# Kernel tuning notes

Hardware: AMD Instinct MI355X
Metric: run time of the kernel (lower is better)

The kernel has to match this reference:

```python
import jax, jax.numpy as jnp
import numpy as np

SEQ_LEN = 181
N_FEAT = 12
N_EMB = 128
N_LAYER = 2
BATCH = 4096


def setup_inputs() -> dict:
    key = jax.random.key(0)
    ks = jax.random.split(key, 13)
    s = 0.05  # small init scale, typical of trained recurrent weights
    H, F = N_EMB, N_FEAT
    return {
        "enc_h": jax.random.normal(ks[0], (N_LAYER, BATCH, H), jnp.float32),
        "enc_c": jax.random.normal(ks[1], (N_LAYER, BATCH, H), jnp.float32),
        "Wih0": jax.random.normal(ks[2], (4 * H, H), jnp.float32) * s,
        "Whh0": jax.random.normal(ks[3], (4 * H, H), jnp.float32) * s,
        "bih0": jax.random.normal(ks[4], (4 * H,), jnp.float32) * s,
        "bhh0": jax.random.normal(ks[5], (4 * H,), jnp.float32) * s,
        "Wih1": jax.random.normal(ks[6], (4 * H, H), jnp.float32) * s,
        "Whh1": jax.random.normal(ks[7], (4 * H, H), jnp.float32) * s,
        "bih1": jax.random.normal(ks[8], (4 * H,), jnp.float32) * s,
        "bhh1": jax.random.normal(ks[9], (4 * H,), jnp.float32) * s,
        "Wout": jax.random.normal(ks[10], (F, N_LAYER * H), jnp.float32) * s,
        "bout": jax.random.normal(ks[11], (F,), jnp.float32) * s,
    }


def _lstm_cell(x, h, c, Wih, Whh, bih, bhh):
    # PyTorch gate order: i, f, g, o
    g = x @ Wih.T + bih + h @ Whh.T + bhh  # (N, 4H)
    i, f, gg, o = jnp.split(g, 4, axis=-1)
    c = jax.nn.sigmoid(f) * c + jax.nn.sigmoid(i) * jnp.tanh(gg)
    h = jax.nn.sigmoid(o) * jnp.tanh(c)
    return h, c


def reference(enc_h, enc_c, Wih0, Whh0, bih0, bhh0, Wih1, Whh1, bih1, bhh1, Wout, bout):
    N, H = enc_h.shape[1], enc_h.shape[2]
    layers = ((Wih0, Whh0, bih0, bhh0), (Wih1, Whh1, bih1, bhh1))

    def lstm2(x_seq, h, c):
        # x_seq: (N, 2, H) batch_first; h, c: (2, N, H)
        inp = x_seq
        hs, cs = [], []
        for l, (Wih, Whh, bih, bhh) in enumerate(layers):
            hl, cl = h[l], c[l]
            outs = []
            for t in range(N_LAYER):  # the fake 'sequence' length equals n_layer=2
                hl, cl = _lstm_cell(inp[:, t], hl, cl, Wih, Whh, bih, bhh)
                outs.append(hl)
            inp = jnp.stack(outs, axis=1)  # (N, 2, H)
            hs.append(hl)
            cs.append(cl)
        return inp, jnp.stack(hs), jnp.stack(cs)

    def step(carry, _):
        dec_in, h, c = carry
        oi, h, c = lstm2(dec_in, h, c)
        out = jax.nn.sigmoid(oi.reshape(N, -1) @ Wout.T + bout)  # (N, n_feat)
        return (oi, h, c), out

    dec_in0 = jnp.zeros((N, N_LAYER, H), enc_h.dtype)
    _, outs = jax.lax.scan(step, (dec_in0, enc_h, enc_c), None, length=SEQ_LEN)
    return jnp.transpose(outs, (1, 0, 2))  # (N, seq_len, n_feat)
```

## Files before the change

### kernel.cpp

```cpp
#include <hip/hip_runtime.h>
#include <hip/hip_bf16.h>

typedef __attribute__((ext_vector_type(8))) short bf16x8;
typedef __attribute__((ext_vector_type(4))) float f32x4;

#define NBATCH 4096
#define SEQT 181
#define NFEAT 12
#define HDIM 128
#define ROWS 16
#define LSTR 136
#define OUTSTRIDE (SEQT*NFEAT)

#define WFRAG_ELEMS 262144
#define WOUT_ELEMS  4096
#define BIAS_F32OFF (532480/4)
#define BOUT_F32OFF (536576/4)
#define BBF16_U16OFF 268320

#define ACT_OFF  131072
#define BIAS_OFF 157184
#define BOUT_OFF 161280
#define SMEM_BYTES 161344

#define SSIG (-1.442695041f)
#define STANH (-2.885390082f)

#define FBAR() asm volatile("s_waitcnt lgkmcnt(0)\n\ts_barrier" ::: "memory")

__device__ __forceinline__ float fsig2(float xs) {
  return __builtin_amdgcn_rcpf(1.0f + __builtin_amdgcn_exp2f(xs));
}
__device__ __forceinline__ unsigned short f2bf(float x) {
  __hip_bfloat16 h = __float2bfloat16(x);
  return __builtin_bit_cast(unsigned short, h);
}

__global__ void setup_kernel(const float* __restrict__ Wih0, const float* __restrict__ Whh0,
                             const float* __restrict__ bih0, const float* __restrict__ bhh0,
                             const float* __restrict__ Wih1, const float* __restrict__ Whh1,
                             const float* __restrict__ bih1, const float* __restrict__ bhh1,
                             const float* __restrict__ Wo,   const float* __restrict__ bo,
                             unsigned short* __restrict__ ws)
{
  int idx = blockIdx.x * blockDim.x + threadIdx.x;
  if (idx < WFRAG_ELEMS) {
    int e = idx & 7, lane = (idx >> 3) & 63, s = (idx >> 9) & 7, g = (idx >> 12) & 3,
        w = (idx >> 14) & 7, l = idx >> 17;
    int row = g * 128 + w * 16 + (lane & 15);
    int k   = s * 32 + (lane >> 4) * 8 + e;
    const float* Wih = l ? Wih1 : Wih0;
    const float* Whh = l ? Whh1 : Whh0;
    float v = (k < HDIM) ? Wih[row * HDIM + k] : Whh[row * HDIM + (k - HDIM)];
    float sc = (g == 2) ? STANH : SSIG;
    ws[idx] = f2bf(v * sc);
  } else if (idx < WFRAG_ELEMS + WOUT_ELEMS) {
    int i2 = idx - WFRAG_ELEMS;
    int e = i2 & 7, lane = (i2 >> 3) & 63, s = i2 >> 9;
    int c = lane & 15;
    int k = s * 32 + (lane >> 4) * 8 + e;
    float v = (c < NFEAT) ? Wo[c * 256 + k] * SSIG : 0.0f;
    ws[idx] = f2bf(v);
  } else if (idx < WFRAG_ELEMS + WOUT_ELEMS + 1024) {
    int i3 = idx - (WFRAG_ELEMS + WOUT_ELEMS);
    int l = i3 >> 9, r = i3 & 511;
    float v = l ? (bih1[r] + bhh1[r]) : (bih0[r] + bhh0[r]);
    reinterpret_cast<float*>(ws)[BIAS_F32OFF + i3] = v;
  } else if (idx < WFRAG_ELEMS + WOUT_ELEMS + 1024 + 16) {
    int i4 = idx - (WFRAG_ELEMS + WOUT_ELEMS + 1024);
    reinterpret_cast<float*>(ws)[BOUT_F32OFF + i4] = (i4 < NFEAT) ? bo[i4] * SSIG : 0.0f;
  } else if (idx < WFRAG_ELEMS + WOUT_ELEMS + 1024 + 16 + 1024) {
    int i5 = idx - (WFRAG_ELEMS + WOUT_ELEMS + 1024 + 16);
    int l = i5 >> 9, r = i5 & 511;
    int w = r >> 6, lg = (r >> 4) & 3, j16 = r & 15;
    int f = j16 >> 3, j = j16 & 7;
    int gate = f * 2 + (j >> 2);
    int dim  = w * 16 + lg * 4 + (j & 3);
    float v = l ? (bih1[gate * 128 + dim] + bhh1[gate * 128 + dim])
                : (bih0[gate * 128 + dim] + bhh0[gate * 128 + dim]);
    float sc = (gate == 2) ? STANH : SSIG;
    ws[BBF16_U16OFF + i5] = f2bf(v * sc);
  }
}

__global__ void
__attribute__((amdgpu_flat_work_group_size(512, 512), amdgpu_waves_per_eu(2, 2)))
lstm_kernel(
    const float* __restrict__ ench, const float* __restrict__ encc,
    const unsigned short* __restrict__ wfrag, const unsigned short* __restrict__ woutf,
    const unsigned short* __restrict__ biasbf, const float* __restrict__ boutc,
    float* __restrict__ out)
{
  __shared__ __align__(16) unsigned char smem[SMEM_BYTES];
  bf16x8* wlds = reinterpret_cast<bf16x8*>(smem);
  unsigned short* act = reinterpret_cast<unsigned short*>(smem + ACT_OFF);

  const int tid  = threadIdx.x;
  const int wave = tid >> 6, lane = tid & 63;
  const int col  = lane & 15, lg = lane >> 4;
  const int n0   = blockIdx.x * ROWS;
  const int dbase = wave * 16 + lg * 4;

  const bf16x8* wfv = reinterpret_cast<const bf16x8*>(wfrag);

  bf16x8 wreg[2][4][6];
  #pragma unroll
  for (int l = 0; l < 2; ++l)
    #pragma unroll
    for (int g = 0; g < 4; ++g) {
      #pragma unroll
      for (int s = 0; s < 6; ++s)
        wreg[l][g][s] = wfv[(size_t)((((l * 8 + wave) * 4 + g) * 8) + s) * 64 + lane];
      #pragma unroll
      for (int s = 0; s < 6; ++s) {
        f32x4 t_ = __builtin_bit_cast(f32x4, wreg[l][g][s]);
        asm volatile("" : "+v"(t_));
        wreg[l][g][s] = __builtin_bit_cast(bf16x8, t_);
      }
      __builtin_amdgcn_sched_barrier(0);
    }

  #pragma unroll
  for (int l = 0; l < 2; ++l)
    #pragma unroll
    for (int g = 0; g < 4; ++g)
      #pragma unroll
      for (int si = 0; si < 2; ++si)
        wlds[(((wave * 2 + l) * 4 + g) * 2 + si) * 64 + lane] =
            wfv[(size_t)((((l * 8 + wave) * 4 + g) * 8) + 6 + si) * 64 + lane];

  for (int i = tid; i < 2 * ROWS * LSTR; i += 512) act[i] = 0;
  for (int i = tid; i < ROWS * HDIM; i += 512) {
    int r = i >> 7, d = i & (HDIM - 1);
    act[(5 * ROWS + r) * LSTR + d] = f2bf(ench[(n0 + r) * HDIM + d]);
    act[(3 * ROWS + r) * LSTR + d] = f2bf(ench[(size_t)(NBATCH + n0 + r) * HDIM + d]);
  }
  for (int i = tid; i < 1024; i += 512)
    reinterpret_cast<unsigned short*>(smem + BIAS_OFF)[i] = biasbf[i];
  if (tid < 16) reinterpret_cast<float*>(smem + BOUT_OFF)[tid] = boutc[tid];
  f32x4 c0 = *reinterpret_cast<const f32x4*>(&encc[(size_t)(n0 + col) * HDIM + dbase]);
  f32x4 c1 = *reinterpret_cast<const f32x4*>(&encc[(size_t)(NBATCH + n0 + col) * HDIM + dbase]);
  __syncthreads();

  const int aoffl = col * LSTR + lg * 8;

  auto cellNB = [&](int xb, int hb, int ob, const bf16x8 (&wr)[4][6], int lb, int bl, f32x4& c) {
    const unsigned short* xp = act + xb * (ROWS * LSTR) + aoffl;
    const unsigned short* hp = act + hb * (ROWS * LSTR) + aoffl;
    const unsigned char* bptr = smem + BIAS_OFF + (size_t)(((bl * 8 + wave) * 4 + lg) * 32);
    bf16x8 bb0 = *reinterpret_cast<const bf16x8*>(bptr);
    bf16x8 bb1 = *reinterpret_cast<const bf16x8*>(bptr + 16);
    f32x4 acc0, acc1, acc2, acc3;
    #pragma unroll
    for (int j = 0; j < 4; ++j) {
      acc0[j] = __builtin_bit_cast(float, ((unsigned)(unsigned short)bb0[j]) << 16);
      acc1[j] = __builtin_bit_cast(float, ((unsigned)(unsigned short)bb0[4 + j]) << 16);
      acc2[j] = __builtin_bit_cast(float, ((unsigned)(unsigned short)bb1[j]) << 16);
      acc3[j] = __builtin_bit_cast(float, ((unsigned)(unsigned short)bb1[4 + j]) << 16);
    }
    #pragma unroll
    for (int s = 0; s < 4; ++s) {
      bf16x8 b = *reinterpret_cast<const bf16x8*>(&xp[s * 32]);
      acc0 = __builtin_amdgcn_mfma_f32_16x16x32_bf16(wr[0][s], b, acc0, 0, 0, 0);
      acc1 = __builtin_amdgcn_mfma_f32_16x16x32_bf16(wr[1][s], b, acc1, 0, 0, 0);
      acc2 = __builtin_amdgcn_mfma_f32_16x16x32_bf16(wr[2][s], b, acc2, 0, 0, 0);
      acc3 = __builtin_amdgcn_mfma_f32_16x16x32_bf16(wr[3][s], b, acc3, 0, 0, 0);
    }
    #pragma unroll
    for (int s = 0; s < 2; ++s) {
      bf16x8 b = *reinterpret_cast<const bf16x8*>(&hp[s * 32]);
      acc0 = __builtin_amdgcn_mfma_f32_16x16x32_bf16(wr[0][4 + s], b, acc0, 0, 0, 0);
      acc1 = __builtin_amdgcn_mfma_f32_16x16x32_bf16(wr[1][4 + s], b, acc1, 0, 0, 0);
      acc2 = __builtin_amdgcn_mfma_f32_16x16x32_bf16(wr[2][4 + s], b, acc2, 0, 0, 0);
      acc3 = __builtin_amdgcn_mfma_f32_16x16x32_bf16(wr[3][4 + s], b, acc3, 0, 0, 0);
    }
    #pragma unroll
    for (int si = 0; si < 2; ++si) {
      bf16x8 b = *reinterpret_cast<const bf16x8*>(&hp[(2 + si) * 32]);
      bf16x8 w0 = wlds[(lb + 0 * 2 + si) * 64 + lane];
      bf16x8 w1 = wlds[(lb + 1 * 2 + si) * 64 + lane];
      bf16x8 w2 = wlds[(lb + 2 * 2 + si) * 64 + lane];
      bf16x8 w3 = wlds[(lb + 3 * 2 + si) * 64 + lane];
      acc0 = __builtin_amdgcn_mfma_f32_16x16x32_bf16(w0, b, acc0, 0, 0, 0);
      acc1 = __builtin_amdgcn_mfma_f32_16x16x32_bf16(w1, b, acc1, 0, 0, 0);
      acc2 = __builtin_amdgcn_mfma_f32_16x16x32_bf16(w2, b, acc2, 0, 0, 0);
      acc3 = __builtin_amdgcn_mfma_f32_16x16x32_bf16(w3, b, acc3, 0, 0, 0);
    }
    unsigned int hu[4];
    #pragma unroll
    for (int j = 0; j < 4; ++j) {
      float Ei = __builtin_amdgcn_exp2f(acc0[j]);
      float Ef = __builtin_amdgcn_exp2f(acc1[j]);
      float Eg = __builtin_amdgcn_exp2f(fminf(acc2[j], 80.0f));
      float Eo = __builtin_amdgcn_exp2f(acc3[j]);
      float sf = __builtin_amdgcn_rcpf(1.0f + Ef);
      float rig = __builtin_amdgcn_rcpf((1.0f + Ei) * (1.0f + Eg));
      float cn = __builtin_fmaf(c[j], sf, (1.0f - Eg) * rig);
      c[j] = cn;
      float Ec = __builtin_amdgcn_exp2f(fminf(STANH * cn, 80.0f));
      float rr = __builtin_amdgcn_rcpf((1.0f + Eo) * (1.0f + Ec));
      hu[j] = f2bf((1.0f - Ec) * rr);
    }
    uint2* op = reinterpret_cast<uint2*>(act + ob * (ROWS * LSTR) + col * LSTR + dbase);
    *op = make_uint2(hu[0] | (hu[1] << 16), hu[2] | (hu[3] << 16));
  };

  const int lb0 = (wave * 2 + 0) * 8;
  const int lb1 = (wave * 2 + 1) * 8;
  const bf16x8* wov = reinterpret_cast<const bf16x8*>(woutf);

  auto outproj = [&](int b0, int b1, int tt) {
    const unsigned short* z0 = act + b0 * (ROWS * LSTR) + aoffl;
    const unsigned short* z1 = act + b1 * (ROWS * LSTR) + aoffl;
    f32x4 po = *reinterpret_cast<const f32x4*>(smem + BOUT_OFF + lg * 16);
    #pragma unroll
    for (int s = 0; s < 4; ++s) {
      bf16x8 z = *reinterpret_cast<const bf16x8*>(&z0[s * 32]);
      po = __builtin_amdgcn_mfma_f32_16x16x32_bf16(wov[s * 64 + lane], z, po, 0, 0, 0);
    }
    #pragma unroll
    for (int s = 0; s < 4; ++s) {
      bf16x8 z = *reinterpret_cast<const bf16x8*>(&z1[s * 32]);
      po = __builtin_amdgcn_mfma_f32_16x16x32_bf16(wov[(4 + s) * 64 + lane], z, po, 0, 0, 0);
    }
    if (lg < 3) {
      f32x4 r;
      r[0] = fsig2(po[0]); r[1] = fsig2(po[1]); r[2] = fsig2(po[2]); r[3] = fsig2(po[3]);
      *reinterpret_cast<f32x4*>(&out[(size_t)(n0 + col) * OUTSTRIDE + tt * NFEAT + lg * 4]) = r;
    }
  };

  cellNB(0, 5, 4, wreg[0], lb0, 0, c0);
  FBAR();

  for (int t = 0; t < SEQT; ++t) {
    const int xA = (t & 1) ? 2 : 0, xB = xA + 1;
    const int zA = (t & 1) ? 0 : 2, zB = zA + 1;
    cellNB(xB, 4, 5, wreg[0], lb0, 0, c0);
    __builtin_amdgcn_sched_barrier(0);
    cellNB(4, (t == 0) ? 3 : xB, zA, wreg[1], lb1, 1, c1);
    if (wave == 0 && t > 0) outproj(xA, xB, t - 1);
    FBAR();
    cellNB(5, zA, zB, wreg[1], lb1, 1, c1);
    __builtin_amdgcn_sched_barrier(0);
    if (t + 1 < SEQT)
      cellNB(zA, 5, 4, wreg[0], lb0, 0, c0);
    FBAR();
  }
  if (wave == 0) outproj(2, 3, SEQT - 1);
}

extern "C" void kernel_launch(void* const* d_in, const int* in_sizes, int n_in,
                              void* d_out, int out_size, void* d_ws, size_t ws_size,
                              hipStream_t stream) {
  const float* ench = (const float*)d_in[0];
  const float* encc = (const float*)d_in[1];
  const float* Wih0 = (const float*)d_in[2];
  const float* Whh0 = (const float*)d_in[3];
  const float* bih0 = (const float*)d_in[4];
  const float* bhh0 = (const float*)d_in[5];
  const float* Wih1 = (const float*)d_in[6];
  const float* Whh1 = (const float*)d_in[7];
  const float* bih1 = (const float*)d_in[8];
  const float* bhh1 = (const float*)d_in[9];
  const float* Wo   = (const float*)d_in[10];
  const float* bo   = (const float*)d_in[11];
  unsigned short* ws = (unsigned short*)d_ws;

  int total = WFRAG_ELEMS + WOUT_ELEMS + 1024 + 16 + 1024;
  int blocks = (total + 511) / 512;
  hipLaunchKernelGGL(setup_kernel, dim3(blocks), dim3(512), 0, stream,
                     Wih0, Whh0, bih0, bhh0, Wih1, Whh1, bih1, bhh1, Wo, bo, ws);

  const unsigned short* wfrag  = ws;
  const unsigned short* woutf  = ws + WFRAG_ELEMS;
  const unsigned short* biasbf = ws + BBF16_U16OFF;
  const float* boutc = reinterpret_cast<const float*>(ws) + BOUT_F32OFF;

  hipLaunchKernelGGL(lstm_kernel, dim3(NBATCH / ROWS), dim3(512), 0, stream,
                     ench, encc, wfrag, woutf, biasbf, boutc, (float*)d_out);
}
```

Before: 791.6 us.

## Fuse paired LSTM cells into one interleaved MFMA stream sharing activation loads

Measured after the change: 991.6 us. +25.3%, slower.

```diff
diff --git a/kernel.cpp b/kernel.cpp
--- a/kernel.cpp
+++ b/kernel.cpp
@@ -27,6 +27,7 @@
 #define STANH (-2.885390082f)
 
 #define FBAR() asm volatile("s_waitcnt lgkmcnt(0)\n\ts_barrier" ::: "memory")
+#define MF(W,B,C) __builtin_amdgcn_mfma_f32_16x16x32_bf16((W),(B),(C),0,0,0)
 
 __device__ __forceinline__ float fsig2(float xs) {
   return __builtin_amdgcn_rcpf(1.0f + __builtin_amdgcn_exp2f(xs));
@@ -34,6 +35,9 @@
 __device__ __forceinline__ unsigned short f2bf(float x) {
   __hip_bfloat16 h = __float2bfloat16(x);
   return __builtin_bit_cast(unsigned short, h);
+}
+__device__ __forceinline__ float bf2f(short u) {
+  return __builtin_bit_cast(float, ((unsigned)(unsigned short)u) << 16);
 }
 
 __global__ void setup_kernel(const float* __restrict__ Wih0, const float* __restrict__ Whh0,
@@ -143,56 +147,21 @@
   __syncthreads();
 
   const int aoffl = col * LSTR + lg * 8;
-
-  auto cellNB = [&](int xb, int hb, int ob, const bf16x8 (&wr)[4][6], int lb, int bl, f32x4& c) {
-    const unsigned short* xp = act + xb * (ROWS * LSTR) + aoffl;
-    const unsigned short* hp = act + hb * (ROWS * LSTR) + aoffl;
+  const int lb0 = (wave * 2 + 0) * 8;
+  const int lb1 = (wave * 2 + 1) * 8;
+  const bf16x8* wov = reinterpret_cast<const bf16x8*>(woutf);
+
+  auto tail = [&](f32x4& a0, f32x4& a1, f32x4& a2, f32x4& a3, int bl, int ob, f32x4& c) {
     const unsigned char* bptr = smem + BIAS_OFF + (size_t)(((bl * 8 + wave) * 4 + lg) * 32);
     bf16x8 bb0 = *reinterpret_cast<const bf16x8*>(bptr);
     bf16x8 bb1 = *reinterpret_cast<const bf16x8*>(bptr + 16);
-    f32x4 acc0, acc1, acc2, acc3;
+    unsigned int hu[4];
     #pragma unroll
     for (int j = 0; j < 4; ++j) {
-      acc0[j] = __builtin_bit_cast(float, ((unsigned)(unsigned short)bb0[j]) << 16);
-      acc1[j] = __builtin_bit_cast(float, ((unsigned)(unsigned short)bb0[4 + j]) << 16);
-      acc2[j] = __builtin_bit_cast(float, ((unsigned)(unsigned short)bb1[j]) << 16);
-      acc3[j] = __builtin_bit_cast(float, ((unsigned)(unsigned short)bb1[4 + j]) << 16);
-    }
-    #pragma unroll
-    for (int s = 0; s < 4; ++s) {
-      bf16x8 b = *reinterpret_cast<const bf16x8*>(&xp[s * 32]);
-      acc0 = __builtin_amdgcn_mfma_f32_16x16x32_bf16(wr[0][s], b, acc0, 0, 0, 0);
-      acc1 = __builtin_amdgcn_mfma_f32_16x16x32_bf16(wr[1][s], b, acc1, 0, 0, 0);
-      acc2 = __builtin_amdgcn_mfma_f32_16x16x32_bf16(wr[2][s], b, acc2, 0, 0, 0);
-      acc3 = __builtin_amdgcn_mfma_f32_16x16x32_bf16(wr[3][s], b, acc3, 0, 0, 0);
-    }
-    #pragma unroll
-    for (int s = 0; s < 2; ++s) {
-      bf16x8 b = *reinterpret_cast<const bf16x8*>(&hp[s * 32]);
-      acc0 = __builtin_amdgcn_mfma_f32_16x16x32_bf16(wr[0][4 + s], b, acc0, 0, 0, 0);
-      acc1 = __builtin_amdgcn_mfma_f32_16x16x32_bf16(wr[1][4 + s], b, acc1, 0, 0, 0);
-      acc2 = __builtin_amdgcn_mfma_f32_16x16x32_bf16(wr[2][4 + s], b, acc2, 0, 0, 0);
-      acc3 = __builtin_amdgcn_mfma_f32_16x16x32_bf16(wr[3][4 + s], b, acc3, 0, 0, 0);
-    }
-    #pragma unroll
-    for (int si = 0; si < 2; ++si) {
-      bf16x8 b = *reinterpret_cast<const bf16x8*>(&hp[(2 + si) * 32]);
-      bf16x8 w0 = wlds[(lb + 0 * 2 + si) * 64 + lane];
-      bf16x8 w1 = wlds[(lb + 1 * 2 + si) * 64 + lane];
-      bf16x8 w2 = wlds[(lb + 2 * 2 + si) * 64 + lane];
-      bf16x8 w3 = wlds[(lb + 3 * 2 + si) * 64 + lane];
-      acc0 = __builtin_amdgcn_mfma_f32_16x16x32_bf16(w0, b, acc0, 0, 0, 0);
-      acc1 = __builtin_amdgcn_mfma_f32_16x16x32_bf16(w1, b, acc1, 0, 0, 0);
-      acc2 = __builtin_amdgcn_mfma_f32_16x16x32_bf16(w2, b, acc2, 0, 0, 0);
-      acc3 = __builtin_amdgcn_mfma_f32_16x16x32_bf16(w3, b, acc3, 0, 0, 0);
-    }
-    unsigned int hu[4];
-    #pragma unroll
-    for (int j = 0; j < 4; ++j) {
-      float Ei = __builtin_amdgcn_exp2f(acc0[j]);
-      float Ef = __builtin_amdgcn_exp2f(acc1[j]);
-      float Eg = __builtin_amdgcn_exp2f(fminf(acc2[j], 80.0f));
-      float Eo = __builtin_amdgcn_exp2f(acc3[j]);
+      float Ei = __builtin_amdgcn_exp2f(a0[j] + bf2f(bb0[j]));
+      float Ef = __builtin_amdgcn_exp2f(a1[j] + bf2f(bb0[4 + j]));
+      float Eg = __builtin_amdgcn_exp2f(fminf(a2[j] + bf2f(bb1[j]), 80.0f));
+      float Eo = __builtin_amdgcn_exp2f(a3[j] + bf2f(bb1[4 + j]));
       float sf = __builtin_amdgcn_rcpf(1.0f + Ef);
       float rig = __builtin_amdgcn_rcpf((1.0f + Ei) * (1.0f + Eg));
       float cn = __builtin_fmaf(c[j], sf, (1.0f - Eg) * rig);
@@ -205,9 +174,93 @@
     *op = make_uint2(hu[0] | (hu[1] << 16), hu[2] | (hu[3] << 16));
   };
 
-  const int lb0 = (wave * 2 + 0) * 8;
-  const int lb1 = (wave * 2 + 1) * 8;
-  const bf16x8* wov = reinterpret_cast<const bf16x8*>(woutf);
+  auto cellNB = [&](int xb, int hb, int ob, const bf16x8 (&wr)[4][6], int lb, int bl, f32x4& c) {
+    const unsigned short* xp = act + xb * (ROWS * LSTR) + aoffl;
+    const unsigned short* hp = act + hb * (ROWS * LSTR) + aoffl;
+    const f32x4 z4 = {0.f, 0.f, 0.f, 0.f};
+    f32x4 A0, A1, A2, A3;
+    {
+      bf16x8 b = *reinterpret_cast<const bf16x8*>(&xp[0]);
+      A0 = MF(wr[0][0], b, z4); A1 = MF(wr[1][0], b, z4);
+      A2 = MF(wr[2][0], b, z4); A3 = MF(wr[3][0], b, z4);
+    }
+    #pragma unroll
+    for (int s = 1; s < 4; ++s) {
+      bf16x8 b = *reinterpret_cast<const bf16x8*>(&xp[s * 32]);
+      A0 = MF(wr[0][s], b, A0); A1 = MF(wr[1][s], b, A1);
+      A2 = MF(wr[2][s], b, A2); A3 = MF(wr[3][s], b, A3);
+    }
+    #pragma unroll
+    for (int s = 0; s < 2; ++s) {
+      bf16x8 b = *reinterpret_cast<const bf16x8*>(&hp[s * 32]);
+      A0 = MF(wr[0][4 + s], b, A0); A1 = MF(wr[1][4 + s], b, A1);
+      A2 = MF(wr[2][4 + s], b, A2); A3 = MF(wr[3][4 + s], b, A3);
+    }
+    #pragma unroll
+    for (int si = 0; si < 2; ++si) {
+      bf16x8 b = *reinterpret_cast<const bf16x8*>(&hp[(2 + si) * 32]);
+      bf16x8 w;
+      w = wlds[(lb + 0 + si) * 64 + lane]; A0 = MF(w, b, A0);
+      w = wlds[(lb + 2 + si) * 64 + lane]; A1 = MF(w, b, A1);
+      w = wlds[(lb + 4 + si) * 64 + lane]; A2 = MF(w, b, A2);
+      w = wlds[(lb + 6 + si) * 64 + lane]; A3 = MF(w, b, A3);
+    }
+    tail(A0, A1, A2, A3, bl, ob, c);
+  };
+
+  auto fusedPair = [&](int pb, int qb,
+                       const bf16x8 (&wrA)[4][6], const bf16x8 (&wrB)[4][6],
+                       int lbA, int lbB, int blA, int blB, int obA, int obB,
+                       f32x4& cA, f32x4& cB) {
+    const unsigned short* pp = act + pb * (ROWS * LSTR) + aoffl;
+    const unsigned short* qp = act + qb * (ROWS * LSTR) + aoffl;
+    const f32x4 z4 = {0.f, 0.f, 0.f, 0.f};
+    f32x4 A0, A1, A2, A3, B0, B1, B2, B3;
+    {
+      bf16x8 fp = *reinterpret_cast<const bf16x8*>(&pp[0]);
+      A0 = MF(wrA[0][0], fp, z4); A1 = MF(wrA[1][0], fp, z4);
+      A2 = MF(wrA[2][0], fp, z4); A3 = MF(wrA[3][0], fp, z4);
+      B0 = MF(wrB[0][4], fp, z4); B1 = MF(wrB[1][4], fp, z4);
+      B2 = MF(wrB[2][4], fp, z4); B3 = MF(wrB[3][4], fp, z4);
+      bf16x8 fq = *reinterpret_cast<const bf16x8*>(&qp[0]);
+      B0 = MF(wrB[0][0], fq, B0); B1 = MF(wrB[1][0], fq, B1);
+      B2 = MF(wrB[2][0], fq, B2); B3 = MF(wrB[3][0], fq, B3);
+      A0 = MF(wrA[0][4], fq, A0); A1 = MF(wrA[1][4], fq, A1);
+      A2 = MF(wrA[2][4], fq, A2); A3 = MF(wrA[3][4], fq, A3);
+    }
+    {
+      bf16x8 fp = *reinterpret_cast<const bf16x8*>(&pp[32]);
+      A0 = MF(wrA[0][1], fp, A0); A1 = MF(wrA[1][1], fp, A1);
+      A2 = MF(wrA[2][1], fp, A2); A3 = MF(wrA[3][1], fp, A3);
+      B0 = MF(wrB[0][5], fp, B0); B1 = MF(wrB[1][5], fp, B1);
+      B2 = MF(wrB[2][5], fp, B2); B3 = MF(wrB[3][5], fp, B3);
+      bf16x8 fq = *reinterpret_cast<const bf16x8*>(&qp[32]);
+      B0 = MF(wrB[0][1], fq, B0); B1 = MF(wrB[1][1], fq, B1);
+      B2 = MF(wrB[2][1], fq, B2); B3 = MF(wrB[3][1], fq, B3);
+      A0 = MF(wrA[0][5], fq, A0); A1 = MF(wrA[1][5], fq, A1);
+      A2 = MF(wrA[2][5], fq, A2); A3 = MF(wrA[3][5], fq, A3);
+    }
+    #pragma unroll
+    for (int si = 0; si < 2; ++si) {
+      bf16x8 fp = *reinterpret_cast<const bf16x8*>(&pp[(2 + si) * 32]);
+      A0 = MF(wrA[0][2 + si], fp, A0); A1 = MF(wrA[1][2 + si], fp, A1);
+      A2 = MF(wrA[2][2 + si], fp, A2); A3 = MF(wrA[3][2 + si], fp, A3);
+      bf16x8 w;
+      w = wlds[(lbB + 0 + si) * 64 + lane]; B0 = MF(w, fp, B0);
+      w = wlds[(lbB + 2 + si) * 64 + lane]; B1 = MF(w, fp, B1);
+      w = wlds[(lbB + 4 + si) * 64 + lane]; B2 = MF(w, fp, B2);
+      w = wlds[(lbB + 6 + si) * 64 + lane]; B3 = MF(w, fp, B3);
+      bf16x8 fq = *reinterpret_cast<const bf16x8*>(&qp[(2 + si) * 32]);
+      B0 = MF(wrB[0][2 + si], fq, B0); B1 = MF(wrB[1][2 + si], fq, B1);
+      B2 = MF(wrB[2][2 + si], fq, B2); B3 = MF(wrB[3][2 + si], fq, B3);
+      w = wlds[(lbA + 0 + si) * 64 + lane]; A0 = MF(w, fq, A0);
+      w = wlds[(lbA + 2 + si) * 64 + lane]; A1 = MF(w, fq, A1);
+      w = wlds[(lbA + 4 + si) * 64 + lane]; A2 = MF(w, fq, A2);
+      w = wlds[(lbA + 6 + si) * 64 + lane]; A3 = MF(w, fq, A3);
+    }
+    tail(A0, A1, A2, A3, blA, obA, cA);
+    tail(B0, B1, B2, B3, blB, obB, cB);
+  };
 
   auto outproj = [&](int b0, int b1, int tt) {
     const unsigned short* z0 = act + b0 * (ROWS * LSTR) + aoffl;
@@ -216,12 +269,12 @@
     #pragma unroll
     for (int s = 0; s < 4; ++s) {
       bf16x8 z = *reinterpret_cast<const bf16x8*>(&z0[s * 32]);
-      po = __builtin_amdgcn_mfma_f32_16x16x32_bf16(wov[s * 64 + lane], z, po, 0, 0, 0);
+      po = MF(wov[s * 64 + lane], z, po);
     }
     #pragma unroll
     for (int s = 0; s < 4; ++s) {
       bf16x8 z = *reinterpret_cast<const bf16x8*>(&z1[s * 32]);
-      po = __builtin_amdgcn_mfma_f32_16x16x32_bf16(wov[(4 + s) * 64 + lane], z, po, 0, 0, 0);
+      po = MF(wov[(4 + s) * 64 + lane], z, po);
     }
     if (lg < 3) {
       f32x4 r;
@@ -232,19 +285,24 @@
 
   cellNB(0, 5, 4, wreg[0], lb0, 0, c0);
   FBAR();
-
-  for (int t = 0; t < SEQT; ++t) {
+  cellNB(1, 4, 5, wreg[0], lb0, 0, c0);
+  __builtin_amdgcn_sched_barrier(0);
+  cellNB(4, 3, 2, wreg[1], lb1, 1, c1);
+  FBAR();
+  fusedPair(5, 2, wreg[1], wreg[0], lb1, lb0, 1, 0, 3, 4, c1, c0);
+  FBAR();
+
+  for (int t = 1; t < SEQT; ++t) {
     const int xA = (t & 1) ? 2 : 0, xB = xA + 1;
     const int zA = (t & 1) ? 0 : 2, zB = zA + 1;
-    cellNB(xB, 4, 5, wreg[0], lb0, 0, c0);
-    __builtin_amdgcn_sched_barrier(0);
-    cellNB(4, (t == 0) ? 3 : xB, zA, wreg[1], lb1, 1, c1);
-    if (wave == 0 && t > 0) outproj(xA, xB, t - 1);
+    fusedPair(xB, 4, wreg[0], wreg[1], lb0, lb1, 0, 1, 5, zA, c0, c1);
+    if (wave == 0) outproj(xA, xB, t - 1);
     FBAR();
-    cellNB(5, zA, zB, wreg[1], lb1, 1, c1);
-    __builtin_amdgcn_sched_barrier(0);
-    if (t + 1 < SEQT)
-      cellNB(zA, 5, 4, wreg[0], lb0, 0, c0);
+    if (t + 1 < SEQT) {
+      fusedPair(5, zA, wreg[1], wreg[0], lb1, lb0, 1, 0, zB, 4, c1, c0);
+    } else {
+      cellNB(5, zA, zB, wreg[1], lb1, 1, c1);
+    }
     FBAR();
   }
   if (wave == 0) outproj(2, 3, SEQT - 1);
```
